# Optimization experiments

Hardware: AMD Instinct MI355X
Metric: run time of the kernel (lower is better)

The kernel has to match this reference:

```python
import jax, jax.numpy as jnp
import numpy as np

PADDED_NODE_ID = -1
B, N, F = 4096, 128, 64


def setup_inputs() -> dict:
    key = jax.random.key(0)
    k1, k2, k3, k4, k5, k6 = jax.random.split(key, 6)
    src_ids = jax.random.randint(k1, (B, N), 0, 1000, dtype=jnp.int64 if jax.config.jax_enable_x64 else jnp.int32)
    dst_ids = jax.random.randint(k2, (B, N), 0, 1000, dtype=src_ids.dtype)
    w1 = jax.random.normal(k3, (F, 1), dtype=jnp.float32) * 0.1
    b1 = jax.random.normal(k4, (F,), dtype=jnp.float32) * 0.1
    w2 = jax.random.normal(k5, (F, F), dtype=jnp.float32) * 0.1
    b2 = jax.random.normal(k6, (F,), dtype=jnp.float32) * 0.1
    return {"src_neighbour_nodes_ids": src_ids, "dst_neighbour_nodes_ids": dst_ids,
            "w1": w1, "b1": b1, "w2": w2, "b2": b2}


def _pairwise_count(a, b):
    # count[b, i] = #{ j : a[b, i] == b[b, j] }  -- batched histogram via equality
    eq = a[:, :, None] == b[:, None, :]  # [B, N, N] bool
    return eq.sum(axis=-1).astype(jnp.float32)


def _mlp(freq, w1, b1, w2, b2):
    # freq: [B, N, 2] -> Linear(1,F) -> ReLU -> Linear(F,F), then sum over dim 2
    h = freq[..., None] * w1[:, 0] + b1          # [B, N, 2, F]
    h = jax.nn.relu(h)
    out = jnp.einsum('bncf,gf->bncg', h, w2) + b2  # [B, N, 2, F]
    return out.sum(axis=2)                        # [B, N, F]


def reference(src_neighbour_nodes_ids, dst_neighbour_nodes_ids, w1, b1, w2, b2):
    src, dst = src_neighbour_nodes_ids, dst_neighbour_nodes_ids
    src_in_src = _pairwise_count(src, src)
    dst_in_dst = _pairwise_count(dst, dst)
    src_in_dst = _pairwise_count(src, dst)
    dst_in_src = _pairwise_count(dst, src)

    src_pad = (src == PADDED_NODE_ID)[..., None]
    dst_pad = (dst == PADDED_NODE_ID)[..., None]
    source_freq = jnp.where(src_pad, 0.0, jnp.stack([src_in_src, src_in_dst], axis=-1))  # [B,N,2]
    dst_freq = jnp.where(dst_pad, 0.0, jnp.stack([dst_in_dst, dst_in_src], axis=-1))      # [B,N,2]

    src_feat = _mlp(source_freq, w1, b1, w2, b2)
    dst_feat = _mlp(dst_freq, w1, b1, w2, b2)
    return src_feat, dst_feat
```

## Files before the change

kernel.cpp:

```cpp
#include <hip/hip_runtime.h>

#define BATCH 4096
#define NN 128
#define FF 64
#define NC 129
#define HIST 1000
#define PADDED_ID (-1)
#define BPB 4
#define GRID (BATCH / BPB)

__global__ void build_table_kernel(const float* __restrict__ w1,
                                   const float* __restrict__ b1,
                                   const float* __restrict__ w2,
                                   const float* __restrict__ b2,
                                   float* __restrict__ table) {
    int c = blockIdx.x;
    int g = threadIdx.x;
    float cf = (float)c;
    float acc = b2[g];
    #pragma unroll
    for (int f = 0; f < FF; ++f) {
        float h = cf * w1[f] + b1[f];
        h = h > 0.0f ? h : 0.0f;
        acc += h * w2[g * FF + f];
    }
    table[c * FF + g] = acc;
}

__global__ __launch_bounds__(256)
void encode_kernel(const int* __restrict__ src,
                   const int* __restrict__ dst,
                   const float* __restrict__ table,
                   float* __restrict__ out) {
    __shared__ float    s_tab[NC * FF];
    __shared__ unsigned s_hist[HIST];
    __shared__ unsigned s_cnt[2 * NN];

    const int tid = threadIdx.x;

    {
        const float4* tg = (const float4*)table;
        float4* ts = (float4*)s_tab;
        #pragma unroll
        for (int idx = tid; idx < (NC * FF) / 4; idx += 256)
            ts[idx] = tg[idx];
    }

    const int g4 = tid & 15;
    const int n0 = tid >> 4;
    const float4* tab4 = (const float4*)s_tab;

    for (int k = 0; k < BPB; ++k) {
        const int b = blockIdx.x * BPB + k;

        const int my = (tid < NN) ? src[b * NN + tid] : dst[b * NN + (tid - NN)];
        const unsigned inc = (tid < NN) ? 1u : 0x10000u;

        __syncthreads();
        #pragma unroll
        for (int i = tid; i < HIST; i += 256) s_hist[i] = 0u;
        __syncthreads();

        if (my != PADDED_ID && (unsigned)my < HIST)
            atomicAdd(&s_hist[my], inc);
        __syncthreads();

        {
            unsigned h = (my != PADDED_ID && (unsigned)my < HIST) ? s_hist[my] : 0u;
            s_cnt[tid] = h;
        }
        __syncthreads();

        float4* out_src = (float4*)out + (size_t)b * (NN * FF / 4);
        float4* out_dst = out_src + (size_t)BATCH * (NN * FF / 4);
        #pragma unroll
        for (int n = n0; n < NN; n += 16) {
            {
                const unsigned h = s_cnt[n];
                const int c0 = (int)(h & 0xffffu), c1 = (int)(h >> 16);
                float4 v0 = tab4[c0 * (FF / 4) + g4];
                float4 v1 = tab4[c1 * (FF / 4) + g4];
                float4 r;
                r.x = v0.x + v1.x; r.y = v0.y + v1.y;
                r.z = v0.z + v1.z; r.w = v0.w + v1.w;
                out_src[n * (FF / 4) + g4] = r;
            }
            {
                const unsigned h = s_cnt[NN + n];
                const int c0 = (int)(h & 0xffffu), c1 = (int)(h >> 16);
                float4 v0 = tab4[c0 * (FF / 4) + g4];
                float4 v1 = tab4[c1 * (FF / 4) + g4];
                float4 r;
                r.x = v0.x + v1.x; r.y = v0.y + v1.y;
                r.z = v0.z + v1.z; r.w = v0.w + v1.w;
                out_dst[n * (FF / 4) + g4] = r;
            }
        }
    }
}

extern "C" void kernel_launch(void* const* d_in, const int* in_sizes, int n_in,
                              void* d_out, int out_size, void* d_ws, size_t ws_size,
                              hipStream_t stream) {
    const int*   src = (const int*)d_in[0];
    const int*   dst = (const int*)d_in[1];
    const float* w1  = (const float*)d_in[2];
    const float* b1  = (const float*)d_in[3];
    const float* w2  = (const float*)d_in[4];
    const float* b2  = (const float*)d_in[5];
    float* out   = (float*)d_out;
    float* table = (float*)d_ws;

    build_table_kernel<<<NC, FF, 0, stream>>>(w1, b1, w2, b2, table);
    encode_kernel<<<GRID, 256, 0, stream>>>(src, dst, table, out);
}
```

Before: 275.4 us.

## Drop shared-memory table staging and launch one block per batch row

The encode kernel no longer copies the 33KB lookup table into LDS. It reads the table directly from global memory, where it should stay cache-resident, and launches one block per batch element instead of four. Shared memory per block shrinks to about 5KB and launch bounds request 8 blocks per CU, so more blocks can be resident at once and the per-block table copy is gone. The cost is that every gather now goes through L1/L2 rather than LDS.

```diff
diff --git a/kernel.cpp b/kernel.cpp
--- a/kernel.cpp
+++ b/kernel.cpp
@@ -6,8 +6,6 @@
 #define NC 129
 #define HIST 1000
 #define PADDED_ID (-1)
-#define BPB 4
-#define GRID (BATCH / BPB)
 
 __global__ void build_table_kernel(const float* __restrict__ w1,
                                    const float* __restrict__ b1,
@@ -27,74 +25,56 @@
     table[c * FF + g] = acc;
 }
 
-__global__ __launch_bounds__(256)
+__global__ __launch_bounds__(256, 8)
 void encode_kernel(const int* __restrict__ src,
                    const int* __restrict__ dst,
                    const float* __restrict__ table,
                    float* __restrict__ out) {
-    __shared__ float    s_tab[NC * FF];
     __shared__ unsigned s_hist[HIST];
     __shared__ unsigned s_cnt[2 * NN];
 
+    const int b   = blockIdx.x;
     const int tid = threadIdx.x;
 
-    {
-        const float4* tg = (const float4*)table;
-        float4* ts = (float4*)s_tab;
-        #pragma unroll
-        for (int idx = tid; idx < (NC * FF) / 4; idx += 256)
-            ts[idx] = tg[idx];
-    }
+    const int my = (tid < NN) ? src[b * NN + tid] : dst[b * NN + (tid - NN)];
+    const unsigned inc = (tid < NN) ? 1u : 0x10000u;
+    const bool valid = (my != PADDED_ID) && ((unsigned)my < HIST);
+
+    #pragma unroll
+    for (int i = tid; i < HIST; i += 256) s_hist[i] = 0u;
+    __syncthreads();
+
+    if (valid) atomicAdd(&s_hist[my], inc);
+    __syncthreads();
+
+    s_cnt[tid] = valid ? s_hist[my] : 0u;
+    __syncthreads();
 
     const int g4 = tid & 15;
     const int n0 = tid >> 4;
-    const float4* tab4 = (const float4*)s_tab;
+    const float4* __restrict__ tab4 = (const float4*)table;
+    float4* out_src = (float4*)out + (size_t)b * (NN * FF / 4);
+    float4* out_dst = out_src + (size_t)BATCH * (NN * FF / 4);
 
-    for (int k = 0; k < BPB; ++k) {
-        const int b = blockIdx.x * BPB + k;
-
-        const int my = (tid < NN) ? src[b * NN + tid] : dst[b * NN + (tid - NN)];
-        const unsigned inc = (tid < NN) ? 1u : 0x10000u;
-
-        __syncthreads();
-        #pragma unroll
-        for (int i = tid; i < HIST; i += 256) s_hist[i] = 0u;
-        __syncthreads();
-
-        if (my != PADDED_ID && (unsigned)my < HIST)
-            atomicAdd(&s_hist[my], inc);
-        __syncthreads();
-
+    #pragma unroll
+    for (int n = n0; n < NN; n += 16) {
         {
-            unsigned h = (my != PADDED_ID && (unsigned)my < HIST) ? s_hist[my] : 0u;
-            s_cnt[tid] = h;
+            const unsigned h = s_cnt[n];
+            float4 v0 = tab4[(h & 0xffffu) * (FF / 4) + g4];
+            float4 v1 = tab4[(h >> 16)     * (FF / 4) + g4];
+            float4 r;
+            r.x = v0.x + v1.x; r.y = v0.y + v1.y;
+            r.z = v0.z + v1.z; r.w = v0.w + v1.w;
+            out_src[n * (FF / 4) + g4] = r;
         }
-        __syncthreads();
-
-        float4* out_src = (float4*)out + (size_t)b * (NN * FF / 4);
-        float4* out_dst = out_src + (size_t)BATCH * (NN * FF / 4);
-        #pragma unroll
-        for (int n = n0; n < NN; n += 16) {
-            {
-                const unsigned h = s_cnt[n];
-                const int c0 = (int)(h & 0xffffu), c1 = (int)(h >> 16);
-                float4 v0 = tab4[c0 * (FF / 4) + g4];
-                float4 v1 = tab4[c1 * (FF / 4) + g4];
-                float4 r;
-                r.x = v0.x + v1.x; r.y = v0.y + v1.y;
-                r.z = v0.z + v1.z; r.w = v0.w + v1.w;
-                out_src[n * (FF / 4) + g4] = r;
-            }
-            {
-                const unsigned h = s_cnt[NN + n];
-                const int c0 = (int)(h & 0xffffu), c1 = (int)(h >> 16);
-                float4 v0 = tab4[c0 * (FF / 4) + g4];
-                float4 v1 = tab4[c1 * (FF / 4) + g4];
-                float4 r;
-                r.x = v0.x + v1.x; r.y = v0.y + v1.y;
-                r.z = v0.z + v1.z; r.w = v0.w + v1.w;
-                out_dst[n * (FF / 4) + g4] = r;
-            }
+        {
+            const unsigned h = s_cnt[NN + n];
+            float4 v0 = tab4[(h & 0xffffu) * (FF / 4) + g4];
+            float4 v1 = tab4[(h >> 16)     * (FF / 4) + g4];
+            float4 r;
+            r.x = v0.x + v1.x; r.y = v0.y + v1.y;
+            r.z = v0.z + v1.z; r.w = v0.w + v1.w;
+            out_dst[n * (FF / 4) + g4] = r;
         }
     }
 }
@@ -112,5 +92,5 @@
     float* table = (float*)d_ws;
 
     build_table_kernel<<<NC, FF, 0, stream>>>(w1, b1, w2, b2, table);
-    encode_kernel<<<GRID, 256, 0, stream>>>(src, dst, table, out);
+    encode_kernel<<<BATCH, 256, 0, stream>>>(src, dst, table, out);
 }
```

New measurement: 275.1 us. About the same (-0.1%).
